# Kernel tuning notes

Measured on AMD Instinct MI355X. Metric: run time of the kernel, lower is better.

Reference implementation:

```python
import math
import jax, jax.numpy as jnp
import numpy as np

LAM = 1.0
TAU = 0.0
BETA0 = -2.0 / (math.e + 0.08)  # lower clamp from the paper; 0.5*BETA0 > -1/e, so W is on the principal real branch


def lambertw(y, iters=8):
    """Principal-branch Lambert W via Halley iterations; valid for y > -1/e."""
    w = jnp.log1p(y)  # good initial guess for y > -1 (here y >= 0.5*BETA0 ~ -0.367)
    for _ in range(iters):
        e = jnp.exp(w)
        f = w * e - y
        w = w - f / (e * (w + 1.0) - (w + 2.0) * f / (2.0 * w + 2.0))
    return w


def bce_with_logits(pr, gt):
    # elementwise BCE with logits, reduction='none'
    return jnp.logaddexp(0.0, pr) - pr * gt


def setup_inputs() -> dict:
    key = jax.random.key(0)
    k1, k2 = jax.random.split(key)
    pr = jax.random.normal(k1, (32, 1, 1024, 1024), dtype=jnp.float32)
    gt = jax.random.uniform(k2, (32, 1, 1024, 1024), dtype=jnp.float32)
    return {"pr": pr, "gt": gt}


def reference(pr, gt):
    input_loss = bce_with_logits(pr, gt)
    beta = (input_loss - TAU) / LAM
    y = 0.5 * jnp.maximum(BETA0, beta)
    # scipy lambertw is outside the autograd graph in the original; sigma is a constant weight
    sigma = jax.lax.stop_gradient(jnp.exp(-lambertw(y)))
    loss = sigma * (input_loss - TAU) + LAM * jnp.log(sigma) ** 2
    return loss
```

## Files before the change

### kernel.cpp

```cpp
#include <hip/hip_runtime.h>
#include <math.h>


__device__ __forceinline__ float superloss_elem(float pr, float gt) {
    float t  = __expf(-fabsf(pr));
    float il = fmaxf(pr, 0.0f) - pr * gt + __logf(1.0f + t);

    float y = 0.5f * il;
    float w = __logf(1.0f + y);

#pragma unroll
    for (int it = 0; it < 2; ++it) {
        float e   = __expf(w);
        float f   = __fmaf_rn(w, e, -y);
        float wp1 = w + 1.0f;
        float num = 2.0f * f * wp1;
        float den = __fmaf_rn(2.0f * e, wp1 * wp1, -(w + 2.0f) * f);
        w = __fmaf_rn(-num, __builtin_amdgcn_rcpf(den), w);
    }
    return w * (w + 2.0f);
}

__global__ __launch_bounds__(256) void superloss_vec4(const float4* __restrict__ pr,
                                                      const float4* __restrict__ gt,
                                                      float4* __restrict__ out,
                                                      int n4) {
    int i = blockIdx.x * blockDim.x + threadIdx.x;
    if (i < n4) {
        float4 p = pr[i];
        float4 g = gt[i];
        float4 o;
        o.x = superloss_elem(p.x, g.x);
        o.y = superloss_elem(p.y, g.y);
        o.z = superloss_elem(p.z, g.z);
        o.w = superloss_elem(p.w, g.w);
        out[i] = o;
    }
}

__global__ __launch_bounds__(256) void superloss_scalar(const float* __restrict__ pr,
                                                        const float* __restrict__ gt,
                                                        float* __restrict__ out,
                                                        int base, int n) {
    int i = base + blockIdx.x * blockDim.x + threadIdx.x;
    if (i < n) {
        out[i] = superloss_elem(pr[i], gt[i]);
    }
}

extern "C" void kernel_launch(void* const* d_in, const int* in_sizes, int n_in,
                              void* d_out, int out_size, void* d_ws, size_t ws_size,
                              hipStream_t stream) {
    const float* pr = (const float*)d_in[0];
    const float* gt = (const float*)d_in[1];
    float* out = (float*)d_out;
    int n = in_sizes[0];

    int n4 = n / 4;
    if (n4 > 0) {
        int blocks = (n4 + 255) / 256;
        superloss_vec4<<<blocks, 256, 0, stream>>>((const float4*)pr, (const float4*)gt,
                                                   (float4*)out, n4);
    }
    int rem = n - n4 * 4;
    if (rem > 0) {
        superloss_scalar<<<1, 256, 0, stream>>>(pr, gt, out, n4 * 4, n);
    }
}
```

Before: 301.5 us.

## Replace Halley exp calls with Taylor-updated exponent, Newton step, vec8 nontemporal stores

The math is reworked so the first Halley step reuses exp(log1p(y)) = 1+y, and the second iteration's exponential comes from a 4th-order Taylor update of the previous exp, followed by a Newton step instead of Halley. Exp and log now use the raw exp2/log2 hardware builtins. Each thread now handles 8 elements with two 16-byte loads per input and writes its outputs with nontemporal stores. This cuts transcendental instruction count and per-thread overhead, at the cost of some accuracy from the Taylor approximation and the lower-order final step.

```diff
diff --git a/kernel.cpp b/kernel.cpp
--- a/kernel.cpp
+++ b/kernel.cpp
@@ -2,40 +2,67 @@
 #include <math.h>
 
 
+typedef float f32x4 __attribute__((ext_vector_type(4)));
+
 __device__ __forceinline__ float superloss_elem(float pr, float gt) {
-    float t  = __expf(-fabsf(pr));
-    float il = fmaxf(pr, 0.0f) - pr * gt + __logf(1.0f + t);
+    const float LOG2E = 1.44269504f;
+    const float LN2   = 0.69314718f;
 
-    float y = 0.5f * il;
-    float w = __logf(1.0f + y);
+    float t  = __builtin_amdgcn_exp2f(-fabsf(pr) * LOG2E);
+    float lg = __builtin_amdgcn_logf(1.0f + t);
+    float il = __fmaf_rn(-pr, gt, fmaxf(pr, 0.0f));
+    il = __fmaf_rn(LN2, lg, il);
 
-#pragma unroll
-    for (int it = 0; it < 2; ++it) {
-        float e   = __expf(w);
-        float f   = __fmaf_rn(w, e, -y);
-        float wp1 = w + 1.0f;
-        float num = 2.0f * f * wp1;
-        float den = __fmaf_rn(2.0f * e, wp1 * wp1, -(w + 2.0f) * f);
-        w = __fmaf_rn(-num, __builtin_amdgcn_rcpf(den), w);
-    }
-    return w * (w + 2.0f);
+    float y   = 0.5f * il;
+    float opy = 1.0f + y;
+    float w0  = LN2 * __builtin_amdgcn_logf(opy);
+
+    float f   = __fmaf_rn(w0, opy, -y);
+    float wp1 = w0 + 1.0f;
+    float num = 2.0f * f * wp1;
+    float den = __fmaf_rn(opy + opy, wp1 * wp1, -(w0 + 2.0f) * f);
+    float w1  = __fmaf_rn(-num, __builtin_amdgcn_rcpf(den), w0);
+
+    float nd = w1 - w0;
+    float p  = __fmaf_rn(nd, 0.041666668f, 0.16666667f);
+    p = __fmaf_rn(nd, p, 0.5f);
+    p = __fmaf_rn(nd, p, 1.0f);
+    p = __fmaf_rn(nd, p, 1.0f);
+    float e = opy * p;
+
+    float f2 = __fmaf_rn(w1, e, -y);
+    float d2 = e * (w1 + 1.0f);
+    float w  = __fmaf_rn(-f2, __builtin_amdgcn_rcpf(d2), w1);
+
+    float u = w + 1.0f;
+    return __fmaf_rn(u, u, -1.0f);
 }
 
-__global__ __launch_bounds__(256) void superloss_vec4(const float4* __restrict__ pr,
-                                                      const float4* __restrict__ gt,
-                                                      float4* __restrict__ out,
-                                                      int n4) {
+__global__ __launch_bounds__(256) void superloss_vec8(const f32x4* __restrict__ pr,
+                                                      const f32x4* __restrict__ gt,
+                                                      f32x4* __restrict__ out,
+                                                      int n8) {
     int i = blockIdx.x * blockDim.x + threadIdx.x;
-    if (i < n4) {
-        float4 p = pr[i];
-        float4 g = gt[i];
-        float4 o;
-        o.x = superloss_elem(p.x, g.x);
-        o.y = superloss_elem(p.y, g.y);
-        o.z = superloss_elem(p.z, g.z);
-        o.w = superloss_elem(p.w, g.w);
-        out[i] = o;
-    }
+    if (i >= n8) return;
+    int b = 2 * i;
+
+    f32x4 p0 = pr[b];
+    f32x4 p1 = pr[b + 1];
+    f32x4 g0 = gt[b];
+    f32x4 g1 = gt[b + 1];
+
+    f32x4 o0, o1;
+    o0.x = superloss_elem(p0.x, g0.x);
+    o0.y = superloss_elem(p0.y, g0.y);
+    o0.z = superloss_elem(p0.z, g0.z);
+    o0.w = superloss_elem(p0.w, g0.w);
+    o1.x = superloss_elem(p1.x, g1.x);
+    o1.y = superloss_elem(p1.y, g1.y);
+    o1.z = superloss_elem(p1.z, g1.z);
+    o1.w = superloss_elem(p1.w, g1.w);
+
+    __builtin_nontemporal_store(o0, out + b);
+    __builtin_nontemporal_store(o1, out + b + 1);
 }
 
 __global__ __launch_bounds__(256) void superloss_scalar(const float* __restrict__ pr,
@@ -56,14 +83,14 @@
     float* out = (float*)d_out;
     int n = in_sizes[0];
 
-    int n4 = n / 4;
-    if (n4 > 0) {
-        int blocks = (n4 + 255) / 256;
-        superloss_vec4<<<blocks, 256, 0, stream>>>((const float4*)pr, (const float4*)gt,
-                                                   (float4*)out, n4);
+    int n8 = n / 8;
+    if (n8 > 0) {
+        int blocks = (n8 + 255) / 256;
+        superloss_vec8<<<blocks, 256, 0, stream>>>((const f32x4*)pr, (const f32x4*)gt,
+                                                   (f32x4*)out, n8);
     }
-    int rem = n - n4 * 4;
+    int rem = n - n8 * 8;
     if (rem > 0) {
-        superloss_scalar<<<1, 256, 0, stream>>>(pr, gt, out, n4 * 4, n);
+        superloss_scalar<<<1, 256, 0, stream>>>(pr, gt, out, n8 * 8, n);
     }
 }
```

After: 316.9 us. +5.1%, slower.
